# Performance work log

Measured on AMD Instinct MI355X. Metric: run time of the kernel, lower is better.

The kernel has to match this reference:

```python
import jax, jax.numpy as jnp
import numpy as np

N_NODES = 50000
N_EDGES = 625000
F_IN = 128
HIDDEN = 128
N_CLASSES = 64


def setup_inputs() -> dict:
    key = jax.random.key(0)
    ks = jax.random.split(key, 8)
    x = jax.random.normal(ks[0], (N_NODES, F_IN), dtype=jnp.float32)
    edge_index = jax.random.randint(ks[1], (2, N_EDGES), 0, N_NODES, dtype=jnp.int64)
    # GCNConv weights (glorot-ish scale) and biases
    def glorot(k, fan_in, fan_out):
        s = jnp.sqrt(6.0 / (fan_in + fan_out))
        return jax.random.uniform(k, (fan_in, fan_out), minval=-s, maxval=s, dtype=jnp.float32)
    W1 = glorot(ks[2], F_IN, HIDDEN)
    b1 = jnp.zeros((HIDDEN,), dtype=jnp.float32)
    W2 = glorot(ks[3], HIDDEN, HIDDEN)
    b2 = jnp.zeros((HIDDEN,), dtype=jnp.float32)
    Wf = glorot(ks[4], HIDDEN, N_CLASSES)
    bf = jnp.zeros((N_CLASSES,), dtype=jnp.float32)
    return {"x": x, "edge_index": edge_index, "W1": W1, "b1": b1,
            "W2": W2, "b2": b2, "Wf": Wf, "bf": bf}


def reference(x, edge_index, W1, b1, W2, b2, Wf, bf):
    # Inference mode: AdaptiveDropout and F.dropout are identity (training=False).
    N = x.shape[0]
    loop = jnp.arange(N, dtype=edge_index.dtype)
    src = jnp.concatenate([edge_index[0], loop])  # source nodes (with self-loops)
    dst = jnp.concatenate([edge_index[1], loop])  # target nodes (with self-loops)
    # Symmetric GCN normalization: deg from edge weights scattered to targets
    deg = jax.ops.segment_sum(jnp.ones(dst.shape[0], dtype=x.dtype), dst, num_segments=N)
    dinv = jnp.where(deg > 0, jax.lax.rsqrt(deg), 0.0)
    norm = dinv[src] * dinv[dst]  # [E+N]

    def gcn(h, W, b):
        m = h @ W                      # [N, out]
        msg = m[src] * norm[:, None]   # gather + scale  [E+N, out]
        return jax.ops.segment_sum(msg, dst, num_segments=N) + b

    h = jax.nn.relu(gcn(x, W1, b1))
    h = jax.nn.relu(gcn(h, W2, b2))
    logits = gcn(h, Wf, bf)
    return jax.nn.log_softmax(logits, axis=1)
```

## Files before the change

kernel.cpp:

```cpp
#include <hip/hip_runtime.h>
#include <cstdint>
#include <cstddef>


#define WAVE 64
#define ELLW 64
typedef _Float16 f16;
typedef f16  f16x4 __attribute__((ext_vector_type(4)));
typedef f16  f16x8 __attribute__((ext_vector_type(8)));
typedef float f32x4 __attribute__((ext_vector_type(4)));


__global__ __launch_bounds__(256) void k_prep(int4* __restrict__ cnt4, int n4,
                                              const float* __restrict__ W1,
                                              const float* __restrict__ W2,
                                              const float* __restrict__ Wf,
                                              f16* __restrict__ Wt1,
                                              f16* __restrict__ Wt2,
                                              f16* __restrict__ Wtf) {
    const int gtid = blockIdx.x * 256 + threadIdx.x;
    const int gsz  = gridDim.x * 256;
    const int4 z = make_int4(0, 0, 0, 0);
    for (int i = gtid; i < n4; i += gsz) cnt4[i] = z;
    for (int i = gtid; i < 40960; i += gsz) {
        if (i < 16384) {
            int n = i >> 7, k = i & 127;
            Wt1[i] = (f16)W1[k * 128 + n];
        } else if (i < 32768) {
            int j = i - 16384;
            int n = j >> 7, k = j & 127;
            Wt2[j] = (f16)W2[k * 128 + n];
        } else {
            int j = i - 32768;
            int n = j >> 7, k = j & 127;
            Wtf[j] = (f16)Wf[k * 64 + n];
        }
    }
}

__global__ void k_fill(const int* __restrict__ src, const int* __restrict__ dst, int E,
                       int* __restrict__ cnt, int* __restrict__ ell, int N) {
    int e = blockIdx.x * blockDim.x + threadIdx.x;
    if (e >= E) return;
    int d = dst[e], s = src[e];
    if ((unsigned)d >= (unsigned)N || (unsigned)s >= (unsigned)N) return;
    int p = atomicAdd(&cnt[d], 1);
    if (p < ELLW) ell[d * ELLW + p] = s;
}

template <int OUT, bool AF32>
__global__ __launch_bounds__(256) void k_gemm_mfma(const void* __restrict__ Av,
                                                   const f16* __restrict__ Wt,
                                                   const int* __restrict__ cnt,
                                                   f16* __restrict__ M,
                                                   int N) {
    constexpr int K  = 128;
    constexpr int CW = OUT / 64;
    __shared__ char smem[OUT * K * 2];
    __shared__ float dl[64];

    const int t    = threadIdx.x;
    const int w    = t >> 6;
    const int lane = t & 63;
    const int ln   = lane & 15;
    const int lh   = lane >> 4;
    const int row0 = blockIdx.x * 64;

    {
        constexpr int NCH = OUT * 16;
        for (int j = t; j < NCH; j += 256) {
            int n = j >> 4;
            uint32_t byte = (uint32_t)j * 16;
            uint32_t swz  = byte ^ (uint32_t)((n & 7) << 4);
            *(f16x8*)(smem + swz) = *(const f16x8*)&Wt[(size_t)j * 8];
        }
        if (t < 64) {
            int r = row0 + t;
            dl[t] = rsqrtf((float)(cnt[r < N ? r : (N - 1)] + 1));
        }
    }
    __syncthreads();

    f16x8 bfr[CW][4];
    const int c0 = w * CW;
#pragma unroll
    for (int c = 0; c < CW; ++c) {
        int n = (c0 + c) * 16 + ln;
#pragma unroll
        for (int q = 0; q < 4; ++q) {
            uint32_t byte = (uint32_t)(n * 256 + q * 64 + lh * 16);
            uint32_t swz  = byte ^ (uint32_t)((n & 7) << 4);
            bfr[c][q] = *(const f16x8*)(smem + swz);
        }
    }
    __syncthreads();

    f32x4 acc[4][CW];
#pragma unroll
    for (int s = 0; s < 4; ++s)
#pragma unroll
        for (int c = 0; c < CW; ++c)
            acc[s][c] = f32x4{0.f, 0.f, 0.f, 0.f};

#pragma unroll
    for (int s = 0; s < 4; ++s) {
        int m = row0 + s * 16 + ln;
        const size_t mrow = (size_t)(m < N ? m : (N - 1)) * K;
#pragma unroll
        for (int q = 0; q < 4; ++q) {
            f16x8 a;
            if constexpr (AF32) {
                const float* ap = (const float*)Av + mrow + q * 32 + lh * 8;
                float4 x0 = *(const float4*)ap;
                float4 x1 = *(const float4*)(ap + 4);
                a = f16x8{ (f16)x0.x, (f16)x0.y, (f16)x0.z, (f16)x0.w,
                           (f16)x1.x, (f16)x1.y, (f16)x1.z, (f16)x1.w };
            } else {
                a = *(const f16x8*)((const f16*)Av + mrow + q * 32 + lh * 8);
            }
#pragma unroll
            for (int c = 0; c < CW; ++c)
                acc[s][c] = __builtin_amdgcn_mfma_f32_16x16x32_f16(a, bfr[c][q], acc[s][c], 0, 0, 0);
        }
    }

    f16* ot = (f16*)smem;
#pragma unroll
    for (int s = 0; s < 4; ++s) {
#pragma unroll
        for (int c = 0; c < CW; ++c) {
            int col = (c0 + c) * 16 + ln;
#pragma unroll
            for (int r = 0; r < 4; ++r) {
                int rl = s * 16 + lh * 4 + r;
                ot[rl * OUT + col] = (f16)(acc[s][c][r] * dl[rl]);
            }
        }
    }
    __syncthreads();

    constexpr int CPR = OUT / 8;
    for (int j = t; j < 64 * CPR; j += 256) {
        int rl = j / CPR;
        if (row0 + rl < N)
            *(f16x8*)&M[(size_t)(row0 + rl) * OUT + (j % CPR) * 8] =
                *(const f16x8*)&ot[(size_t)j * 8];
    }
}

__global__ __launch_bounds__(256) void k_agg128_f16(const f16* __restrict__ M16,
                                                    const int* __restrict__ ell,
                                                    const int* __restrict__ cnt,
                                                    const float* __restrict__ bias,
                                                    f16* __restrict__ H16, int N) {
    const int lane = threadIdx.x & (WAVE - 1);
    const int sub  = lane >> 5;
    const int q    = (lane & 31) >> 4;
    const int fl   = lane & 15;
    const int fo   = fl * 8;
    const int node = blockIdx.x * 8 + ((threadIdx.x >> 6) << 1) + sub;
    if (node >= N) return;

    float a[8] = {0.f, 0.f, 0.f, 0.f, 0.f, 0.f, 0.f, 0.f};
    if (q == 0) {
        f16x8 v = *(const f16x8*)&M16[(size_t)node * 128 + fo];
#pragma unroll
        for (int i = 0; i < 8; ++i) a[i] = (float)v[i];
    }

    const int deg = cnt[node];
    const int e1  = deg < ELLW ? deg : ELLW;
    const int* erow = ell + (size_t)node * ELLW;
    for (int base = 0; base < e1; base += 16) {
        int   s[8];
        float w[8];
#pragma unroll
        for (int j = 0; j < 8; ++j) {
            int i = base + 2 * j + q;
            bool ok = i < e1;
            s[j] = erow[ok ? i : 0];
            w[j] = ok ? 1.f : 0.f;
        }
        f16x8 v[8];
#pragma unroll
        for (int j = 0; j < 8; ++j)
            v[j] = *(const f16x8*)&M16[(size_t)s[j] * 128 + fo];
#pragma unroll
        for (int j = 0; j < 8; ++j)
#pragma unroll
            for (int i = 0; i < 8; ++i)
                a[i] += w[j] * (float)v[j][i];
    }

#pragma unroll
    for (int i = 0; i < 8; ++i) a[i] += __shfl_xor(a[i], 16);

    if (q == 0) {
        const float dn = rsqrtf((float)(deg + 1));
        float4 b0 = *(const float4*)&bias[fo];
        float4 b1 = *(const float4*)&bias[fo + 4];
        f16x8 o;
        o[0] = (f16)fmaxf(a[0] * dn + b0.x, 0.f);
        o[1] = (f16)fmaxf(a[1] * dn + b0.y, 0.f);
        o[2] = (f16)fmaxf(a[2] * dn + b0.z, 0.f);
        o[3] = (f16)fmaxf(a[3] * dn + b0.w, 0.f);
        o[4] = (f16)fmaxf(a[4] * dn + b1.x, 0.f);
        o[5] = (f16)fmaxf(a[5] * dn + b1.y, 0.f);
        o[6] = (f16)fmaxf(a[6] * dn + b1.z, 0.f);
        o[7] = (f16)fmaxf(a[7] * dn + b1.w, 0.f);
        *(f16x8*)&H16[(size_t)node * 128 + fo] = o;
    }
}

__global__ __launch_bounds__(256) void k_agg64_lsm(const f16* __restrict__ M16,
                                                   const int* __restrict__ ell,
                                                   const int* __restrict__ cnt,
                                                   const float* __restrict__ bias,
                                                   float* __restrict__ Y, int N) {
    const int lane = threadIdx.x & (WAVE - 1);
    const int sub  = lane >> 5;
    const int q    = (lane & 31) >> 4;
    const int fl   = lane & 15;
    const int fo   = fl * 4;
    const int node = blockIdx.x * 8 + ((threadIdx.x >> 6) << 1) + sub;
    if (node >= N) return;

    float a[4] = {0.f, 0.f, 0.f, 0.f};
    if (q == 0) {
        f16x4 v = *(const f16x4*)&M16[(size_t)node * 64 + fo];
#pragma unroll
        for (int i = 0; i < 4; ++i) a[i] = (float)v[i];
    }

    const int deg = cnt[node];
    const int e1  = deg < ELLW ? deg : ELLW;
    const int* erow = ell + (size_t)node * ELLW;
    for (int base = 0; base < e1; base += 16) {
        int   s[8];
        float w[8];
#pragma unroll
        for (int j = 0; j < 8; ++j) {
            int i = base + 2 * j + q;
            bool ok = i < e1;
            s[j] = erow[ok ? i : 0];
            w[j] = ok ? 1.f : 0.f;
        }
        f16x4 v[8];
#pragma unroll
        for (int j = 0; j < 8; ++j)
            v[j] = *(const f16x4*)&M16[(size_t)s[j] * 64 + fo];
#pragma unroll
        for (int j = 0; j < 8; ++j)
#pragma unroll
            for (int i = 0; i < 4; ++i)
                a[i] += w[j] * (float)v[j][i];
    }

#pragma unroll
    for (int i = 0; i < 4; ++i) a[i] += __shfl_xor(a[i], 16);

    const float dn = rsqrtf((float)(deg + 1));
    float4 b = *(const float4*)&bias[fo];
    float v0 = a[0] * dn + b.x;
    float v1 = a[1] * dn + b.y;
    float v2 = a[2] * dn + b.z;
    float v3 = a[3] * dn + b.w;
    float m = fmaxf(fmaxf(v0, v1), fmaxf(v2, v3));
#pragma unroll
    for (int o = 8; o > 0; o >>= 1) m = fmaxf(m, __shfl_xor(m, o));
    float s = expf(v0 - m) + expf(v1 - m) + expf(v2 - m) + expf(v3 - m);
#pragma unroll
    for (int o = 8; o > 0; o >>= 1) s += __shfl_xor(s, o);
    if (q == 0) {
        float ls = logf(s);
        float4 o4 = make_float4(v0 - m - ls, v1 - m - ls, v2 - m - ls, v3 - m - ls);
        *(float4*)&Y[(size_t)node * 64 + fo] = o4;
    }
}


extern "C" void kernel_launch(void* const* d_in, const int* in_sizes, int n_in,
                              void* d_out, int out_size, void* d_ws, size_t ws_size,
                              hipStream_t stream) {
    const float* x  = (const float*)d_in[0];
    const int*   ei = (const int*)d_in[1];
    const float* W1 = (const float*)d_in[2];
    const float* b1 = (const float*)d_in[3];
    const float* W2 = (const float*)d_in[4];
    const float* b2 = (const float*)d_in[5];
    const float* Wf = (const float*)d_in[6];
    const float* bf = (const float*)d_in[7];
    float* out = (float*)d_out;

    const int N = in_sizes[0] / 128;
    const int E = in_sizes[1] / 2;
    const int* srcv = ei;
    const int* dstv = ei + E;

    char* ws = (char*)d_ws;
    auto alloc = [&](size_t bytes) -> void* {
        void* p = ws;
        ws += (bytes + 255) & ~(size_t)255;
        return p;
    };
    int*   cnt    = (int*)alloc((size_t)N * 4 + 16);
    int*   ell    = (int*)alloc((size_t)N * ELLW * 4);
    f16*   m16    = (f16*)alloc((size_t)N * 128 * 2);
    f16*   h16    = (f16*)alloc((size_t)N * 128 * 2);
    f16*   Wt1    = (f16*)alloc(128 * 128 * 2);
    f16*   Wt2    = (f16*)alloc(128 * 128 * 2);
    f16*   Wtf    = (f16*)alloc(128 * 64 * 2);

    const int TB = 256;
    const int n4 = (N + 3) / 4;

    k_prep<<<224, TB, 0, stream>>>((int4*)cnt, n4, W1, W2, Wf, Wt1, Wt2, Wtf);
    k_fill<<<(E + TB - 1) / TB, TB, 0, stream>>>(srcv, dstv, E, cnt, ell, N);

    const int gemm_grid = (N + 63) / 64;
    const int agg_grid  = (N + 7) / 8;

    k_gemm_mfma<128, true><<<gemm_grid, 256, 0, stream>>>(x, Wt1, cnt, m16, N);
    k_agg128_f16<<<agg_grid, 256, 0, stream>>>(m16, ell, cnt, b1, h16, N);

    k_gemm_mfma<128, false><<<gemm_grid, 256, 0, stream>>>(h16, Wt2, cnt, m16, N);
    k_agg128_f16<<<agg_grid, 256, 0, stream>>>(m16, ell, cnt, b2, h16, N);

    k_gemm_mfma<64, false><<<gemm_grid, 256, 0, stream>>>(h16, Wtf, cnt, m16, N);
    k_agg64_lsm<<<agg_grid, 256, 0, stream>>>(m16, ell, cnt, bf, out, N);
}
```

Measured before the change: 162.2 us.

## Build ELL adjacency via sharded 16-node buckets then per-bucket LDS scatter

Replaces the single-pass atomic scatter of edges into per-node ELL rows with two passes. The first pass appends packed (local-dst, src) entries into sharded 16-node buckets. The second pass builds each bucket's ELL rows and counts with shared-memory atomics. This is meant to cut global atomic contention and the scattered 4-byte writes across the large ELL array, at the cost of an extra kernel launch and an intermediate buffer. Packing src into 16 bits only holds when N is at most 65536, and bucket overflow past BCAP silently drops edges.

```diff
diff --git a/kernel.cpp b/kernel.cpp
--- a/kernel.cpp
+++ b/kernel.cpp
@@ -5,13 +5,15 @@
 
 #define WAVE 64
 #define ELLW 64
+#define NSH  8
+#define BCAP 96
 typedef _Float16 f16;
 typedef f16  f16x4 __attribute__((ext_vector_type(4)));
 typedef f16  f16x8 __attribute__((ext_vector_type(8)));
 typedef float f32x4 __attribute__((ext_vector_type(4)));
 
 
-__global__ __launch_bounds__(256) void k_prep(int4* __restrict__ cnt4, int n4,
+__global__ __launch_bounds__(256) void k_prep(int4* __restrict__ cur4, int n4,
                                               const float* __restrict__ W1,
                                               const float* __restrict__ W2,
                                               const float* __restrict__ Wf,
@@ -21,7 +23,7 @@
     const int gtid = blockIdx.x * 256 + threadIdx.x;
     const int gsz  = gridDim.x * 256;
     const int4 z = make_int4(0, 0, 0, 0);
-    for (int i = gtid; i < n4; i += gsz) cnt4[i] = z;
+    for (int i = gtid; i < n4; i += gsz) cur4[i] = z;
     for (int i = gtid; i < 40960; i += gsz) {
         if (i < 16384) {
             int n = i >> 7, k = i & 127;
@@ -38,14 +40,55 @@
     }
 }
 
-__global__ void k_fill(const int* __restrict__ src, const int* __restrict__ dst, int E,
-                       int* __restrict__ cnt, int* __restrict__ ell, int N) {
+__global__ void k_bucket(const int* __restrict__ src, const int* __restrict__ dst, int E,
+                         int* __restrict__ cur, int* __restrict__ bsh, int N) {
     int e = blockIdx.x * blockDim.x + threadIdx.x;
     if (e >= E) return;
     int d = dst[e], s = src[e];
     if ((unsigned)d >= (unsigned)N || (unsigned)s >= (unsigned)N) return;
-    int p = atomicAdd(&cnt[d], 1);
-    if (p < ELLW) ell[d * ELLW + p] = s;
+    int b  = d >> 4;
+    int sh = blockIdx.x & (NSH - 1);
+    int p  = atomicAdd(&cur[b * NSH + sh], 1);
+    if (p < BCAP)
+        bsh[(size_t)(b * NSH + sh) * BCAP + p] = ((d & 15) << 16) | s;
+}
+
+__global__ __launch_bounds__(256) void k_build(const int* __restrict__ cur,
+                                               const int* __restrict__ bsh,
+                                               int* __restrict__ ell,
+                                               int* __restrict__ cnt, int N) {
+    __shared__ int lcnt[16];
+    __shared__ int pre[NSH + 1];
+    const int b = blockIdx.x;
+    const int t = threadIdx.x;
+    if (t < 16) lcnt[t] = 0;
+    if (t == 0) {
+        int acc = 0;
+#pragma unroll
+        for (int s2 = 0; s2 < NSH; ++s2) {
+            pre[s2] = acc;
+            int c = cur[b * NSH + s2];
+            acc += (c < BCAP ? c : BCAP);
+        }
+        pre[NSH] = acc;
+    }
+    __syncthreads();
+    const int total = pre[NSH];
+    for (int i = t; i < total; i += 256) {
+        int s2 = 0;
+        while (pre[s2 + 1] <= i) ++s2;
+        int v   = bsh[(size_t)(b * NSH + s2) * BCAP + (i - pre[s2])];
+        int ld  = v >> 16;
+        int sa  = v & 0xFFFF;
+        int slot = atomicAdd(&lcnt[ld], 1);
+        if (slot < ELLW)
+            ell[(size_t)(b * 16 + ld) * ELLW + slot] = sa;
+    }
+    __syncthreads();
+    if (t < 16) {
+        int node = b * 16 + t;
+        if (node < N) cnt[node] = lcnt[t];
+    }
 }
 
 template <int OUT, bool AF32>
@@ -303,7 +346,10 @@
         ws += (bytes + 255) & ~(size_t)255;
         return p;
     };
-    int*   cnt    = (int*)alloc((size_t)N * 4 + 16);
+    const int nbuck = (N + 15) / 16;
+    int*   cur    = (int*)alloc((size_t)nbuck * NSH * 4 + 16);
+    int*   bsh    = (int*)alloc((size_t)nbuck * NSH * BCAP * 4);
+    int*   cnt    = (int*)alloc((size_t)N * 4);
     int*   ell    = (int*)alloc((size_t)N * ELLW * 4);
     f16*   m16    = (f16*)alloc((size_t)N * 128 * 2);
     f16*   h16    = (f16*)alloc((size_t)N * 128 * 2);
@@ -312,10 +358,11 @@
     f16*   Wtf    = (f16*)alloc(128 * 64 * 2);
 
     const int TB = 256;
-    const int n4 = (N + 3) / 4;
-
-    k_prep<<<224, TB, 0, stream>>>((int4*)cnt, n4, W1, W2, Wf, Wt1, Wt2, Wtf);
-    k_fill<<<(E + TB - 1) / TB, TB, 0, stream>>>(srcv, dstv, E, cnt, ell, N);
+    const int n4 = (nbuck * NSH + 3) / 4;
+
+    k_prep<<<224, TB, 0, stream>>>((int4*)cur, n4, W1, W2, Wf, Wt1, Wt2, Wtf);
+    k_bucket<<<(E + TB - 1) / TB, TB, 0, stream>>>(srcv, dstv, E, cur, bsh, N);
+    k_build<<<nbuck, TB, 0, stream>>>(cur, bsh, ell, cnt, N);
 
     const int gemm_grid = (N + 63) / 64;
     const int agg_grid  = (N + 7) / 8;
```

New measurement: 164.7 us. About the same (+1.5%).
